# Optimization experiments

Hardware: AMD Instinct MI355X
Metric: run time of the kernel (lower is better)

The kernel has to match this reference:

```python
import jax, jax.numpy as jnp
import numpy as np

NS, B, T, S, H, V, G = 30, 16, 8, 400, 400, 20000, 3


def setup_inputs() -> dict:
    key = jax.random.key(0)
    ks = jax.random.split(key, 16)
    f = lambda k, shp, s: jax.random.normal(k, shp, jnp.float32) * s
    return dict(
        encoded_hidden=f(ks[0], (B, H), 1.0),
        encoded_outputs=f(ks[1], (B, S, H), 1.0),
        slot_emb=f(ks[2], (NS, H), 0.1),
        emb=f(ks[3], (V, H), 0.1),
        W_ih=f(ks[4], (3 * H, H), 0.05),
        W_hh=f(ks[5], (3 * H, H), 0.05),
        b_ih=jnp.zeros((3 * H,), jnp.float32),
        b_hh=jnp.zeros((3 * H,), jnp.float32),
        W_ratio_w=f(ks[6], (1, 3 * H), 0.05),
        W_ratio_b=jnp.zeros((1,), jnp.float32),
        W_gate_w=f(ks[7], (G, H), 0.05),
        W_gate_b=jnp.zeros((G,), jnp.float32),
        story=jax.random.randint(ks[8], (B, S), 0, V),
        target=jax.random.randint(ks[9], (B, NS, T), 0, V),
        encoded_lens=jax.random.randint(ks[10], (B,), S // 2, S + 1).astype(jnp.int32),
    )


def reference(encoded_hidden, encoded_outputs, slot_emb, emb, W_ih, W_hh, b_ih, b_hh,
              W_ratio_w, W_ratio_b, W_gate_w, W_gate_b, story, target, encoded_lens):
    ns, h = slot_emb.shape
    b, s, _ = encoded_outputs.shape
    t = target.shape[2]
    v = emb.shape[0]
    bs = ns * b  # fused slot*batch decode rows (parallel_decode)

    enc_out = jnp.tile(encoded_outputs, (ns, 1, 1))            # [bs,S,H]
    story_r = jnp.tile(story, (ns, 1))                          # [bs,S]
    lens_r = jnp.tile(encoded_lens, (ns,))                      # [bs]
    mask = jnp.arange(s)[None, :] < lens_r[:, None]             # [bs,S]
    h0 = jnp.tile(encoded_hidden, (ns, 1))                      # [bs,H]
    x0 = jnp.broadcast_to(slot_emb[:, None, :], (ns, b, h)).reshape(bs, h)
    # teacher-forcing inputs, slot-major flatten like target[:, :, wi].T.flatten()
    tf_in = emb[jnp.transpose(target, (2, 1, 0)).reshape(t, bs)]  # [T,bs,H]
    row = jnp.arange(bs)[:, None]
    neg_inf = jnp.float32(-jnp.inf)

    def gru_cell(x, hid):
        gi = x @ W_ih.T + b_ih
        gh = hid @ W_hh.T + b_hh
        ir, iz, inn = jnp.split(gi, 3, axis=-1)
        hr, hz, hn = jnp.split(gh, 3, axis=-1)
        r = jax.nn.sigmoid(ir + hr)
        z = jax.nn.sigmoid(iz + hz)
        n = jnp.tanh(inn + r * hn)
        return (1.0 - z) * n + z * hid

    def step(carry, x_next):
        hid, x = carry
        h_new = gru_cell(x, hid)                                # dec_state == hidden for 1-step GRU
        scores = jnp.einsum('bh,bsh->bs', h_new, enc_out)
        scores = jnp.where(mask, scores, neg_inf)
        prob = jax.nn.softmax(scores, axis=1)
        context = jnp.einsum('bs,bsh->bh', prob, enc_out)
        p_vocab = jax.nn.softmax(h_new @ emb.T, axis=1)         # [bs,V]
        p_gen_vec = jnp.concatenate([h_new, context, x], axis=-1)
        switch = jax.nn.sigmoid(p_gen_vec @ W_ratio_w.T + W_ratio_b)  # [bs,1]
        p_ctx = jnp.zeros((bs, v), p_vocab.dtype).at[row, story_r].add(prob)
        final = (1.0 - switch) * p_ctx + switch * p_vocab
        gate = context @ W_gate_w.T + W_gate_b
        return (h_new, x_next), (final, gate)

    _, (finals, gates) = jax.lax.scan(step, (h0, x0), tf_in)
    all_point = finals.reshape(t, ns, b, v).transpose(1, 2, 0, 3)  # [NS,B,T,V]
    all_gate = gates[0].reshape(ns, b, -1)                          # gates from wi==0
    return all_point, all_gate
```

## Files before the change

### kernel.cpp

```cpp
#include <hip/hip_runtime.h>
#include <hip/hip_bf16.h>

#define NSLOT 30
#define BB    16
#define TT    8
#define SS    400
#define HH    400
#define KP    416
#define NKK   13
#define VV    20000
#define GG    3
#define BSR   480
#define NBN   157
#define NCT   1256
#define NG2   1200
#define NCT2  75
#define NRT   30
#define FRAG_STRIDE 512

typedef unsigned short u16;
typedef __attribute__((ext_vector_type(8))) short bf16x8;
typedef __attribute__((ext_vector_type(4))) float f32x4;

__device__ __forceinline__ short f2bfs(float f){
  __hip_bfloat16 h = __float2bfloat16(f);
  union { __hip_bfloat16 b; short u; } v; v.b = h; return v.u;
}
__device__ __forceinline__ unsigned int pack2(float lo, float hi){
  return (unsigned int)(u16)f2bfs(lo) | ((unsigned int)(u16)f2bfs(hi) << 16);
}
__device__ __forceinline__ float bfu(u16 u){
  union { unsigned int i; float f; } v; v.i = ((unsigned int)u) << 16; return v.f;
}
__device__ __forceinline__ float sigm(float x){ return 1.f / (1.f + __expf(-x)); }
__device__ __forceinline__ float tanh_fast(float x){
  float e = __expf(2.f * x);
  return 1.f - 2.f / (e + 1.f);
}
__device__ __forceinline__ float wred_max(float v){
  #pragma unroll
  for (int off = 32; off; off >>= 1) v = fmaxf(v, __shfl_xor(v, off, 64));
  return v;
}
__device__ __forceinline__ float wred_sum(float v){
  #pragma unroll
  for (int off = 32; off; off >>= 1) v += __shfl_xor(v, off, 64);
  return v;
}

__global__ __launch_bounds__(256) void k_init(const float* __restrict__ eh,
                                              const float* __restrict__ semb,
                                              float* __restrict__ h_ws,
                                              float* __restrict__ x_ws)
{
  int idx = blockIdx.x * 256 + threadIdx.x;
  if (idx >= BSR * HH) return;
  int r = idx / HH, k = idx - r * HH;
  int batch = r % BB, slot = r / BB;
  h_ws[idx] = eh[batch * HH + k];
  x_ws[idx] = semb[slot * HH + k];
}

__global__ __launch_bounds__(256) void k_split_xh(
    const float* __restrict__ h_ws, const float* __restrict__ x_ws,
    short* __restrict__ h_hi, short* __restrict__ h_lo,
    short* __restrict__ x_hi, short* __restrict__ x_lo)
{
  const int NU = NRT * NKK * 64;
  for (int u = blockIdx.x * 256 + threadIdx.x; u < 2 * NU; u += gridDim.x * 256){
    int uu = u; int sel = 0;
    if (uu >= NU){ uu -= NU; sel = 1; }
    const float* S = sel ? x_ws : h_ws;
    short* ph = sel ? x_hi : h_hi;
    short* pl = sel ? x_lo : h_lo;
    int lane = uu & 63, kt = uu >> 6;
    int rtile = kt / NKK, kk = kt - rtile * NKK;
    int lg = lane >> 4, rl = lane & 15;
    int r = rtile * 16 + rl, k = kk * 32 + lg * 8;
    bf16x8 oh, ol;
    #pragma unroll
    for (int j = 0; j < 8; ++j){
      if (k + j < HH){
        float v = S[(size_t)r * HH + k + j];
        short hb = f2bfs(v);
        oh[j] = hb; ol[j] = f2bfs(v - bfu((u16)hb));
      } else { oh[j] = 0; ol[j] = 0; }
    }
    *reinterpret_cast<bf16x8*>(ph + (size_t)uu * 8) = oh;
    *reinterpret_cast<bf16x8*>(pl + (size_t)uu * 8) = ol;
  }
}

__global__ __launch_bounds__(256) void k_cast_W(
    const float* __restrict__ Wih, const float* __restrict__ Whh,
    short* __restrict__ Wih_hi, short* __restrict__ Wih_lo,
    short* __restrict__ Whh_hi, short* __restrict__ Whh_lo)
{
  const int NU = NCT2 * NKK * 64;
  for (int u = blockIdx.x * 256 + threadIdx.x; u < 2 * NU; u += gridDim.x * 256){
    int uu = u; int sel = 0;
    if (uu >= NU){ uu -= NU; sel = 1; }
    const float* W = sel ? Whh : Wih;
    short* ph = sel ? Whh_hi : Wih_hi;
    short* pl = sel ? Whh_lo : Wih_lo;
    int lane = uu & 63, kt = uu >> 6;
    int ctile = kt / NKK, kk = kt - ctile * NKK;
    int lg = lane >> 4, cl = lane & 15;
    int c = ctile * 16 + cl, k = kk * 32 + lg * 8;
    bf16x8 oh, ol;
    #pragma unroll
    for (int j = 0; j < 8; ++j){
      if (k + j < HH){
        float v = W[(size_t)c * HH + k + j];
        short hb = f2bfs(v);
        oh[j] = hb; ol[j] = f2bfs(v - bfu((u16)hb));
      } else { oh[j] = 0; ol[j] = 0; }
    }
    *reinterpret_cast<bf16x8*>(ph + (size_t)uu * 8) = oh;
    *reinterpret_cast<bf16x8*>(pl + (size_t)uu * 8) = ol;
  }
}

__global__ __launch_bounds__(256) void k_cast_emb(const float* __restrict__ emb,
                                                  short* __restrict__ ebf)
{
  const int nunit = NCT * NKK * 64;
  for (int u = blockIdx.x * 256 + threadIdx.x; u < nunit; u += gridDim.x * 256){
    int lane = u & 63;
    int kt = u >> 6;
    int ctile = kt / NKK, kk = kt - ctile * NKK;
    int lg = lane >> 4, cl = lane & 15;
    int c = ctile * 16 + cl;
    int k = kk * 32 + lg * 8;
    bf16x8 o;
    if (c < VV && k < HH){
      const float* src = emb + (size_t)c * HH + k;
      #pragma unroll
      for (int j = 0; j < 8; ++j) o[j] = f2bfs(src[j]);
    } else {
      #pragma unroll
      for (int j = 0; j < 8; ++j) o[j] = 0;
    }
    *reinterpret_cast<bf16x8*>(ebf + (size_t)u * 8) = o;
  }
}

__global__ __launch_bounds__(256) void k_gemm2_mfma(
    const short* __restrict__ x_hi, const short* __restrict__ x_lo,
    const short* __restrict__ h_hi, const short* __restrict__ h_lo,
    const short* __restrict__ Wih_hi, const short* __restrict__ Wih_lo,
    const short* __restrict__ Whh_hi, const short* __restrict__ Whh_lo,
    float* __restrict__ gi, float* __restrict__ gh)
{
  const int t = threadIdx.x;
  const int lane = t & 63, wid = t >> 6;
  const int wr = wid >> 1, wc = wid & 1;
  const int l15 = lane & 15, lg = lane >> 4;
  const int bM = blockIdx.x, bN = blockIdx.y, z = blockIdx.z;

  const short* A_hi = z ? h_hi : x_hi;
  const short* A_lo = z ? h_lo : x_lo;
  const short* B_hi = z ? Whh_hi : Wih_hi;
  const short* B_lo = z ? Whh_lo : Wih_lo;
  float* C = z ? gh : gi;

  const short *ah[4], *al[4], *bh[4], *bl[4];
  #pragma unroll
  for (int m = 0; m < 4; ++m){
    int rtile = min(bM * 8 + wr * 4 + m, NRT - 1);
    size_t off = (size_t)rtile * (NKK * FRAG_STRIDE) + lane * 8;
    ah[m] = A_hi + off; al[m] = A_lo + off;
  }
  #pragma unroll
  for (int n = 0; n < 4; ++n){
    int ctile = min(bN * 8 + wc * 4 + n, NCT2 - 1);
    size_t off = (size_t)ctile * (NKK * FRAG_STRIDE) + lane * 8;
    bh[n] = B_hi + off; bl[n] = B_lo + off;
  }

  f32x4 acc[4][4];
  #pragma unroll
  for (int m = 0; m < 4; ++m)
    #pragma unroll
    for (int n = 0; n < 4; ++n)
      acc[m][n] = (f32x4){0.f, 0.f, 0.f, 0.f};

  #pragma unroll
  for (int kk = 0; kk < NKK; ++kk){
    const int ko = kk * FRAG_STRIDE;
    bf16x8 ah_r[4], al_r[4];
    #pragma unroll
    for (int m = 0; m < 4; ++m){
      ah_r[m] = *reinterpret_cast<const bf16x8*>(ah[m] + ko);
      al_r[m] = *reinterpret_cast<const bf16x8*>(al[m] + ko);
    }
    #pragma unroll
    for (int n = 0; n < 4; ++n){
      bf16x8 bhv = *reinterpret_cast<const bf16x8*>(bh[n] + ko);
      bf16x8 blv = *reinterpret_cast<const bf16x8*>(bl[n] + ko);
      #pragma unroll
      for (int m = 0; m < 4; ++m){
        acc[m][n] = __builtin_amdgcn_mfma_f32_16x16x32_bf16(ah_r[m], bhv, acc[m][n], 0, 0, 0);
        acc[m][n] = __builtin_amdgcn_mfma_f32_16x16x32_bf16(ah_r[m], blv, acc[m][n], 0, 0, 0);
        acc[m][n] = __builtin_amdgcn_mfma_f32_16x16x32_bf16(al_r[m], bhv, acc[m][n], 0, 0, 0);
      }
    }
  }

  #pragma unroll
  for (int m = 0; m < 4; ++m){
    #pragma unroll
    for (int q = 0; q < 4; ++q){
      int row = bM * 128 + wr * 64 + m * 16 + lg * 4 + q;
      if (row < BSR){
        #pragma unroll
        for (int n = 0; n < 4; ++n){
          int col = bN * 128 + wc * 64 + n * 16 + l15;
          if (col < NG2) C[(size_t)row * NG2 + col] = acc[m][n][q];
        }
      }
    }
  }
}

__global__ __launch_bounds__(256) void k_logits_mfma(
    const short* __restrict__ hbf, const short* __restrict__ ebf,
    float* __restrict__ out, float* __restrict__ pmax_ws,
    float* __restrict__ psum_ws, int wi)
{
  const int t = threadIdx.x;
  const int lane = t & 63, wid = t >> 6;
  const int wr = wid >> 1, wc = wid & 1;
  const int l15 = lane & 15, lg = lane >> 4;
  const int bM = blockIdx.x, bN = blockIdx.y;

  const short* ap[4];
  const short* bp[4];
  #pragma unroll
  for (int m = 0; m < 4; ++m){
    int rtile = bM * 8 + wr * 4 + m;
    ap[m] = hbf + (size_t)min(rtile, NRT - 1) * (NKK * FRAG_STRIDE) + lane * 8;
  }
  #pragma unroll
  for (int n = 0; n < 4; ++n){
    int ctile = bN * 8 + wc * 4 + n;
    bp[n] = ebf + (size_t)ctile * (NKK * FRAG_STRIDE) + lane * 8;
  }

  f32x4 acc[4][4];
  #pragma unroll
  for (int m = 0; m < 4; ++m)
    #pragma unroll
    for (int n = 0; n < 4; ++n)
      acc[m][n] = (f32x4){0.f, 0.f, 0.f, 0.f};

  #pragma unroll
  for (int kk = 0; kk < NKK; ++kk){
    const int ko = kk * FRAG_STRIDE;
    bf16x8 a[4];
    #pragma unroll
    for (int m = 0; m < 4; ++m)
      a[m] = *reinterpret_cast<const bf16x8*>(ap[m] + ko);
    #pragma unroll
    for (int n = 0; n < 4; ++n){
      bf16x8 b = *reinterpret_cast<const bf16x8*>(bp[n] + ko);
      #pragma unroll
      for (int m = 0; m < 4; ++m)
        acc[m][n] = __builtin_amdgcn_mfma_f32_16x16x32_bf16(a[m], b, acc[m][n], 0, 0, 0);
    }
  }

  #pragma unroll
  for (int m = 0; m < 4; ++m){
    #pragma unroll
    for (int q = 0; q < 4; ++q){
      int row = bM * 128 + wr * 64 + m * 16 + lg * 4 + q;
      u16* lrow16 = reinterpret_cast<u16*>(out + ((size_t)row * TT + wi) * VV);
      #pragma unroll
      for (int n = 0; n < 4; ++n){
        float v = acc[m][n][q];
        float vp = __shfl_xor(v, 1, 64);
        int col = bN * 128 + wc * 64 + n * 16 + l15;
        if (((l15 & 1) == 0) && row < BSR && col < VV)
          *reinterpret_cast<unsigned int*>(lrow16 + col) = pack2(v, vp);
      }
    }
    f32x4 rmax, rsum;
    #pragma unroll
    for (int q = 0; q < 4; ++q){
      float mx = -3.0e38f;
      #pragma unroll
      for (int n = 0; n < 4; ++n){
        int col = bN * 128 + wc * 64 + n * 16 + l15;
        float v = (col < VV) ? acc[m][n][q] : -3.0e38f;
        mx = fmaxf(mx, v);
      }
      #pragma unroll
      for (int off = 1; off < 16; off <<= 1) mx = fmaxf(mx, __shfl_xor(mx, off, 64));
      float sm = 0.f;
      #pragma unroll
      for (int n = 0; n < 4; ++n){
        int col = bN * 128 + wc * 64 + n * 16 + l15;
        if (col < VV) sm += __expf(acc[m][n][q] - mx);
      }
      #pragma unroll
      for (int off = 1; off < 16; off <<= 1) sm += __shfl_xor(sm, off, 64);
      rmax[q] = mx; rsum[q] = sm;
    }
    if (l15 == 0){
      #pragma unroll
      for (int q = 0; q < 4; ++q){
        int row = bM * 128 + wr * 64 + m * 16 + lg * 4 + q;
        if (row < BSR){
          size_t pidx = ((size_t)row * NBN + bN) * 2 + wc;
          pmax_ws[pidx] = rmax[q];
          psum_ws[pidx] = rsum[q];
        }
      }
    }
  }
}

__global__ __launch_bounds__(256) void k_att(
    const float* __restrict__ enc, const float* __restrict__ emb,
    const float* __restrict__ b_ih, const float* __restrict__ b_hh,
    const float* __restrict__ Wr_w, const float* __restrict__ Wr_b,
    const float* __restrict__ Wg_w, const float* __restrict__ Wg_b,
    const int* __restrict__ target, const int* __restrict__ lens,
    const float* __restrict__ gi_ws, const float* __restrict__ gh_ws,
    float* __restrict__ h_ws, float* __restrict__ x_ws,
    short* __restrict__ h_hi, short* __restrict__ h_lo,
    short* __restrict__ x_hi, short* __restrict__ x_lo,
    float* __restrict__ prob_ws, float* __restrict__ sw_ws,
    float* __restrict__ d_out, int wi)
{
  __shared__ float hn_s[HH];
  __shared__ float sc_s[SS];
  __shared__ float ctx_s[HH];
  __shared__ float red[4];
  __shared__ float redg[GG][4];

  const int t = threadIdx.x;
  const int rg = blockIdx.x;
  const int batch = rg % BB, slot = rg / BB;
  const int len = lens[batch];
  const int rtile = rg >> 4, rl = rg & 15;

  const float* gir = gi_ws + (size_t)rg * NG2;
  const float* ghr = gh_ws + (size_t)rg * NG2;
  for (int k = t; k < HH; k += 256){
    float irv = gir[k]          + b_ih[k];
    float izv = gir[HH + k]     + b_ih[HH + k];
    float inv = gir[2 * HH + k] + b_ih[2 * HH + k];
    float hrv = ghr[k]          + b_hh[k];
    float hzv = ghr[HH + k]     + b_hh[HH + k];
    float hnv = ghr[2 * HH + k] + b_hh[2 * HH + k];
    float rr = sigm(irv + hrv);
    float zz = sigm(izv + hzv);
    float nn = tanh_fast(inv + rr * hnv);
    float hold = h_ws[(size_t)rg * HH + k];
    float hnew = (1.f - zz) * nn + zz * hold;
    hn_s[k] = hnew;
    h_ws[(size_t)rg * HH + k] = hnew;
  }
  __syncthreads();

  if (t < KP / 8){
    const int kk = t >> 2, lg = t & 3;
    bf16x8 oh, ol;
    #pragma unroll
    for (int j = 0; j < 8; ++j){
      int k = t * 8 + j;
      if (k < HH){
        float v = hn_s[k];
        short hb = f2bfs(v);
        oh[j] = hb; ol[j] = f2bfs(v - bfu((u16)hb));
      } else { oh[j] = 0; ol[j] = 0; }
    }
    size_t off = ((size_t)rtile * NKK + kk) * FRAG_STRIDE + (lg * 16 + rl) * 8;
    *reinterpret_cast<bf16x8*>(h_hi + off) = oh;
    *reinterpret_cast<bf16x8*>(h_lo + off) = ol;
  }

  const float* encb = enc + (size_t)batch * SS * HH;
  float lmax = -3.0e38f;
  for (int s = t; s < SS; s += 256){
    if (s < len){
      const float4* er4 = reinterpret_cast<const float4*>(encb + (size_t)s * HH);
      float dot = 0.f;
      for (int k4 = 0; k4 < HH / 4; ++k4){
        float4 e = er4[k4];
        float4 hv = *reinterpret_cast<const float4*>(&hn_s[k4 * 4]);
        dot += e.x*hv.x + e.y*hv.y + e.z*hv.z + e.w*hv.w;
      }
      sc_s[s] = dot;
      lmax = fmaxf(lmax, dot);
    }
  }
  lmax = wred_max(lmax);
  if ((t & 63) == 0) red[t >> 6] = lmax;
  __syncthreads();
  lmax = fmaxf(fmaxf(red[0], red[1]), fmaxf(red[2], red[3]));
  float lsum = 0.f;
  for (int s = t; s < SS; s += 256){
    float e = (s < len) ? __expf(sc_s[s] - lmax) : 0.f;
    sc_s[s] = e;
    lsum += e;
  }
  lsum = wred_sum(lsum);
  __syncthreads();
  if ((t & 63) == 0) red[t >> 6] = lsum;
  __syncthreads();
  lsum = red[0] + red[1] + red[2] + red[3];
  float invl = 1.f / lsum;
  for (int s = t; s < SS; s += 256){
    float p = sc_s[s] * invl;
    sc_s[s] = p;
    prob_ws[(size_t)rg * SS + s] = p;
  }
  __syncthreads();

  for (int k = t; k < HH; k += 256){
    float c0 = 0.f, c1 = 0.f, c2 = 0.f, c3 = 0.f;
    const float* ek = encb + k;
    int s = 0;
    for (; s + 3 < len; s += 4){
      c0 += sc_s[s]     * ek[(size_t)s * HH];
      c1 += sc_s[s + 1] * ek[(size_t)(s + 1) * HH];
      c2 += sc_s[s + 2] * ek[(size_t)(s + 2) * HH];
      c3 += sc_s[s + 3] * ek[(size_t)(s + 3) * HH];
    }
    for (; s < len; ++s) c0 += sc_s[s] * ek[(size_t)s * HH];
    ctx_s[k] = (c0 + c1) + (c2 + c3);
  }
  __syncthreads();

  float sa = 0.f;
  for (int k = t; k < HH; k += 256){
    sa += Wr_w[k]          * hn_s[k]
        + Wr_w[HH + k]     * ctx_s[k]
        + Wr_w[2 * HH + k] * x_ws[(size_t)rg * HH + k];
  }
  sa = wred_sum(sa);
  if ((t & 63) == 0) red[t >> 6] = sa;
  __syncthreads();
  sa = red[0] + red[1] + red[2] + red[3];
  if (t == 0) sw_ws[rg] = sigm(sa + Wr_b[0]);

  if (wi == 0){
    float ga[GG] = {0.f, 0.f, 0.f};
    for (int k = t; k < HH; k += 256){
      float cv = ctx_s[k];
      ga[0] += Wg_w[k] * cv;
      ga[1] += Wg_w[HH + k] * cv;
      ga[2] += Wg_w[2 * HH + k] * cv;
    }
    #pragma unroll
    for (int g = 0; g < GG; ++g){
      ga[g] = wred_sum(ga[g]);
      if ((t & 63) == 0) redg[g][t >> 6] = ga[g];
    }
    __syncthreads();
    if (t < GG)
      d_out[(size_t)NSLOT * BB * TT * VV + (size_t)rg * GG + t] =
          redg[t][0] + redg[t][1] + redg[t][2] + redg[t][3] + Wg_b[t];
  }

  const int tgt = target[batch * (NSLOT * TT) + slot * TT + wi];
  const float* embrow = emb + (size_t)tgt * HH;
  for (int k = t; k < HH; k += 256)
    x_ws[(size_t)rg * HH + k] = embrow[k];
  if (t < KP / 8){
    const int kk = t >> 2, lg = t & 3;
    bf16x8 oh, ol;
    #pragma unroll
    for (int j = 0; j < 8; ++j){
      int k = t * 8 + j;
      if (k < HH){
        float v = embrow[k];
        short hb = f2bfs(v);
        oh[j] = hb; ol[j] = f2bfs(v - bfu((u16)hb));
      } else { oh[j] = 0; ol[j] = 0; }
    }
    size_t off = ((size_t)rtile * NKK + kk) * FRAG_STRIDE + (lg * 16 + rl) * 8;
    *reinterpret_cast<bf16x8*>(x_hi + off) = oh;
    *reinterpret_cast<bf16x8*>(x_lo + off) = ol;
  }
}

__global__ __launch_bounds__(256) void k_finalize(
    float* __restrict__ logits_out, const float* __restrict__ prob_ws,
    const float* __restrict__ pmax_ws, const float* __restrict__ psum_ws,
    const float* __restrict__ sw_ws, const int* __restrict__ story,
    const int* __restrict__ lens, int wi)
{
  __shared__ float pctx[VV];
  __shared__ u16 rowbuf[VV];
  __shared__ float red[4];
  const int t = threadIdx.x;
  const int r = blockIdx.x;
  const int batch = r % BB;
  for (int v = t; v < VV; v += 256) pctx[v] = 0.f;
  __syncthreads();
  const int len = lens[batch];
  for (int s = t; s < SS; s += 256){
    if (s < len)
      atomicAdd(&pctx[story[batch * SS + s]], prob_ws[(size_t)r * SS + s]);
  }

  float* lrow = logits_out + ((size_t)r * TT + wi) * VV;
  const uint4* l16 = reinterpret_cast<const uint4*>(lrow);
  for (int i = t; i < VV / 8; i += 256)
    reinterpret_cast<uint4*>(rowbuf)[i] = l16[i];

  const float* pm = pmax_ws + (size_t)r * (NBN * 2);
  const float* ps = psum_ws + (size_t)r * (NBN * 2);
  float m = -3.0e38f;
  for (int i = t; i < NBN * 2; i += 256) m = fmaxf(m, pm[i]);
  m = wred_max(m);
  if ((t & 63) == 0) red[t >> 6] = m;
  __syncthreads();
  m = fmaxf(fmaxf(red[0], red[1]), fmaxf(red[2], red[3]));
  float lsum = 0.f;
  for (int i = t; i < NBN * 2; i += 256) lsum += ps[i] * __expf(pm[i] - m);
  lsum = wred_sum(lsum);
  __syncthreads();
  if ((t & 63) == 0) red[t >> 6] = lsum;
  __syncthreads();
  lsum = red[0] + red[1] + red[2] + red[3];

  const float sw = sw_ws[r];
  const float invl = sw / lsum;
  const float osw = 1.f - sw;
  float4* o4 = reinterpret_cast<float4*>(lrow);
  for (int i = t; i < VV / 4; i += 256){
    ushort4 s4 = reinterpret_cast<const ushort4*>(rowbuf)[i];
    int v = i * 4;
    float4 o;
    o.x = __expf(bfu(s4.x) - m) * invl + osw * pctx[v + 0];
    o.y = __expf(bfu(s4.y) - m) * invl + osw * pctx[v + 1];
    o.z = __expf(bfu(s4.z) - m) * invl + osw * pctx[v + 2];
    o.w = __expf(bfu(s4.w) - m) * invl + osw * pctx[v + 3];
    o4[i] = o;
  }
}

extern "C" void kernel_launch(void* const* d_in, const int* in_sizes, int n_in,
                              void* d_out, int out_size, void* d_ws, size_t ws_size,
                              hipStream_t stream)
{
  (void)in_sizes; (void)n_in; (void)out_size; (void)ws_size;
  const float* eh    = (const float*)d_in[0];
  const float* enc   = (const float*)d_in[1];
  const float* semb  = (const float*)d_in[2];
  const float* emb   = (const float*)d_in[3];
  const float* W_ih  = (const float*)d_in[4];
  const float* W_hh  = (const float*)d_in[5];
  const float* b_ih  = (const float*)d_in[6];
  const float* b_hh  = (const float*)d_in[7];
  const float* Wr_w  = (const float*)d_in[8];
  const float* Wr_b  = (const float*)d_in[9];
  const float* Wg_w  = (const float*)d_in[10];
  const float* Wg_b  = (const float*)d_in[11];
  const int* story = (const int*)d_in[12];
  const int* tgt   = (const int*)d_in[13];
  const int* lens  = (const int*)d_in[14];
  float* out = (float*)d_out;

  float* ws      = (float*)d_ws;
  float* h_ws    = ws;
  float* x_ws    = ws + 192000;
  float* prob_ws = ws + 384000;
  float* sw_ws   = ws + 576000;
  float* gi_ws   = ws + 576512;
  float* gh_ws   = ws + 1152512;
  float* pmax_ws = ws + 1728512;
  float* psum_ws = ws + 1879552;
  short* h_hi    = (short*)(ws + 2030592);
  short* emb_bf  = (short*)(ws + 2130432);
  short* Wih_hi  = (short*)(ws + 6310400);
  short* Wih_lo  = (short*)(ws + 6560000);
  short* Whh_hi  = (short*)(ws + 6809600);
  short* Whh_lo  = (short*)(ws + 7059200);
  short* x_hi    = (short*)(ws + 7308800);
  short* x_lo    = (short*)(ws + 7408640);
  short* h_lo    = (short*)(ws + 7508480);

  k_cast_emb<<<2048, 256, 0, stream>>>(emb, emb_bf);
  k_cast_W<<<512, 256, 0, stream>>>(W_ih, W_hh, Wih_hi, Wih_lo, Whh_hi, Whh_lo);
  k_init<<<750, 256, 0, stream>>>(eh, semb, h_ws, x_ws);
  k_split_xh<<<195, 256, 0, stream>>>(h_ws, x_ws, h_hi, h_lo, x_hi, x_lo);
  for (int wi = 0; wi < TT; ++wi){
    dim3 gg(4, 10, 2);
    k_gemm2_mfma<<<gg, 256, 0, stream>>>(x_hi, x_lo, h_hi, h_lo,
                                         Wih_hi, Wih_lo, Whh_hi, Whh_lo,
                                         gi_ws, gh_ws);
    k_att<<<BSR, 256, 0, stream>>>(enc, emb, b_ih, b_hh, Wr_w, Wr_b, Wg_w, Wg_b,
                                   tgt, lens, gi_ws, gh_ws, h_ws, x_ws,
                                   h_hi, h_lo, x_hi, x_lo,
                                   prob_ws, sw_ws, out, wi);
    dim3 gl(4, NBN);
    k_logits_mfma<<<gl, 256, 0, stream>>>(h_hi, emb_bf, out, pmax_ws, psum_ws, wi);
    k_finalize<<<BSR, 256, 0, stream>>>(out, prob_ws, pmax_ws, psum_ws,
                                        sw_ws, story, lens, wi);
  }
}
```

Baseline: 1.017 ms.

## Cast encoder outputs to bf16 and split finalize into dense and scatter passes

Encoder outputs are converted once to bf16, and the attention kernel reads the bf16 copy for both the score and context loops, halving the bytes streamed from enc each step. The finalize kernel is split in two. The first writes the scaled vocab softmax without the 80KB shared pctx buffer, which should raise occupancy. The second scatters the copy-distribution probabilities into the output row with global atomics. In exchange, attention precision drops to bf16, there is one more launch per step, and a one-time cast kernel is added.

```diff
diff --git a/kernel.cpp b/kernel.cpp
--- a/kernel.cpp
+++ b/kernel.cpp
@@ -32,6 +32,12 @@
 __device__ __forceinline__ float bfu(u16 u){
   union { unsigned int i; float f; } v; v.i = ((unsigned int)u) << 16; return v.f;
 }
+__device__ __forceinline__ float bfu_lo(unsigned int u){
+  union { unsigned int i; float f; } v; v.i = u << 16; return v.f;
+}
+__device__ __forceinline__ float bfu_hi(unsigned int u){
+  union { unsigned int i; float f; } v; v.i = u & 0xffff0000u; return v.f;
+}
 __device__ __forceinline__ float sigm(float x){ return 1.f / (1.f + __expf(-x)); }
 __device__ __forceinline__ float tanh_fast(float x){
   float e = __expf(2.f * x);
@@ -59,6 +65,14 @@
   int batch = r % BB, slot = r / BB;
   h_ws[idx] = eh[batch * HH + k];
   x_ws[idx] = semb[slot * HH + k];
+}
+
+__global__ __launch_bounds__(256) void k_cast_enc(const float* __restrict__ enc,
+                                                  u16* __restrict__ enc_bf)
+{
+  const int n = BB * SS * HH;
+  for (int i = blockIdx.x * 256 + threadIdx.x; i < n; i += gridDim.x * 256)
+    enc_bf[i] = (u16)f2bfs(enc[i]);
 }
 
 __global__ __launch_bounds__(256) void k_split_xh(
@@ -322,7 +336,7 @@
 }
 
 __global__ __launch_bounds__(256) void k_att(
-    const float* __restrict__ enc, const float* __restrict__ emb,
+    const u16* __restrict__ enc_bf, const float* __restrict__ emb,
     const float* __restrict__ b_ih, const float* __restrict__ b_hh,
     const float* __restrict__ Wr_w, const float* __restrict__ Wr_b,
     const float* __restrict__ Wg_w, const float* __restrict__ Wg_b,
@@ -382,16 +396,19 @@
     *reinterpret_cast<bf16x8*>(h_lo + off) = ol;
   }
 
-  const float* encb = enc + (size_t)batch * SS * HH;
+  const u16* encb = enc_bf + (size_t)batch * SS * HH;
   float lmax = -3.0e38f;
   for (int s = t; s < SS; s += 256){
     if (s < len){
-      const float4* er4 = reinterpret_cast<const float4*>(encb + (size_t)s * HH);
+      const uint4* er4 = reinterpret_cast<const uint4*>(encb + (size_t)s * HH);
       float dot = 0.f;
-      for (int k4 = 0; k4 < HH / 4; ++k4){
-        float4 e = er4[k4];
-        float4 hv = *reinterpret_cast<const float4*>(&hn_s[k4 * 4]);
-        dot += e.x*hv.x + e.y*hv.y + e.z*hv.z + e.w*hv.w;
+      for (int k8 = 0; k8 < HH / 8; ++k8){
+        uint4 e = er4[k8];
+        const float* hv = &hn_s[k8 * 8];
+        dot += bfu_lo(e.x)*hv[0] + bfu_hi(e.x)*hv[1]
+             + bfu_lo(e.y)*hv[2] + bfu_hi(e.y)*hv[3]
+             + bfu_lo(e.z)*hv[4] + bfu_hi(e.z)*hv[5]
+             + bfu_lo(e.w)*hv[6] + bfu_hi(e.w)*hv[7];
       }
       sc_s[s] = dot;
       lmax = fmaxf(lmax, dot);
@@ -422,15 +439,15 @@
 
   for (int k = t; k < HH; k += 256){
     float c0 = 0.f, c1 = 0.f, c2 = 0.f, c3 = 0.f;
-    const float* ek = encb + k;
+    const u16* ek = encb + k;
     int s = 0;
     for (; s + 3 < len; s += 4){
-      c0 += sc_s[s]     * ek[(size_t)s * HH];
-      c1 += sc_s[s + 1] * ek[(size_t)(s + 1) * HH];
-      c2 += sc_s[s + 2] * ek[(size_t)(s + 2) * HH];
-      c3 += sc_s[s + 3] * ek[(size_t)(s + 3) * HH];
-    }
-    for (; s < len; ++s) c0 += sc_s[s] * ek[(size_t)s * HH];
+      c0 += sc_s[s]     * bfu(ek[(size_t)s * HH]);
+      c1 += sc_s[s + 1] * bfu(ek[(size_t)(s + 1) * HH]);
+      c2 += sc_s[s + 2] * bfu(ek[(size_t)(s + 2) * HH]);
+      c3 += sc_s[s + 3] * bfu(ek[(size_t)(s + 3) * HH]);
+    }
+    for (; s < len; ++s) c0 += sc_s[s] * bfu(ek[(size_t)s * HH]);
     ctx_s[k] = (c0 + c1) + (c2 + c3);
   }
   __syncthreads();
@@ -488,25 +505,15 @@
   }
 }
 
-__global__ __launch_bounds__(256) void k_finalize(
-    float* __restrict__ logits_out, const float* __restrict__ prob_ws,
+__global__ __launch_bounds__(256) void k_fin1(
+    float* __restrict__ logits_out,
     const float* __restrict__ pmax_ws, const float* __restrict__ psum_ws,
-    const float* __restrict__ sw_ws, const int* __restrict__ story,
-    const int* __restrict__ lens, int wi)
-{
-  __shared__ float pctx[VV];
+    const float* __restrict__ sw_ws, int wi)
+{
   __shared__ u16 rowbuf[VV];
   __shared__ float red[4];
   const int t = threadIdx.x;
   const int r = blockIdx.x;
-  const int batch = r % BB;
-  for (int v = t; v < VV; v += 256) pctx[v] = 0.f;
-  __syncthreads();
-  const int len = lens[batch];
-  for (int s = t; s < SS; s += 256){
-    if (s < len)
-      atomicAdd(&pctx[story[batch * SS + s]], prob_ws[(size_t)r * SS + s]);
-  }
 
   float* lrow = logits_out + ((size_t)r * TT + wi) * VV;
   const uint4* l16 = reinterpret_cast<const uint4*>(lrow);
@@ -529,20 +536,31 @@
   __syncthreads();
   lsum = red[0] + red[1] + red[2] + red[3];
 
-  const float sw = sw_ws[r];
-  const float invl = sw / lsum;
-  const float osw = 1.f - sw;
+  const float invl = sw_ws[r] / lsum;
   float4* o4 = reinterpret_cast<float4*>(lrow);
   for (int i = t; i < VV / 4; i += 256){
     ushort4 s4 = reinterpret_cast<const ushort4*>(rowbuf)[i];
-    int v = i * 4;
     float4 o;
-    o.x = __expf(bfu(s4.x) - m) * invl + osw * pctx[v + 0];
-    o.y = __expf(bfu(s4.y) - m) * invl + osw * pctx[v + 1];
-    o.z = __expf(bfu(s4.z) - m) * invl + osw * pctx[v + 2];
-    o.w = __expf(bfu(s4.w) - m) * invl + osw * pctx[v + 3];
+    o.x = __expf(bfu(s4.x) - m) * invl;
+    o.y = __expf(bfu(s4.y) - m) * invl;
+    o.z = __expf(bfu(s4.z) - m) * invl;
+    o.w = __expf(bfu(s4.w) - m) * invl;
     o4[i] = o;
   }
+}
+
+__global__ __launch_bounds__(128) void k_fin2(
+    float* __restrict__ logits_out, const float* __restrict__ prob_ws,
+    const float* __restrict__ sw_ws, const int* __restrict__ story,
+    const int* __restrict__ lens, int wi)
+{
+  const int r = blockIdx.x, t = threadIdx.x;
+  const int batch = r % BB;
+  const int len = lens[batch];
+  const float osw = 1.f - sw_ws[r];
+  float* lrow = logits_out + ((size_t)r * TT + wi) * VV;
+  for (int s = t; s < len; s += 128)
+    atomicAdd(&lrow[story[batch * SS + s]], osw * prob_ws[(size_t)r * SS + s]);
 }
 
 extern "C" void kernel_launch(void* const* d_in, const int* in_sizes, int n_in,
@@ -585,9 +603,11 @@
   short* x_hi    = (short*)(ws + 7308800);
   short* x_lo    = (short*)(ws + 7408640);
   short* h_lo    = (short*)(ws + 7508480);
+  u16*   enc_bf  = (u16*)(ws + 7608320);
 
   k_cast_emb<<<2048, 256, 0, stream>>>(emb, emb_bf);
   k_cast_W<<<512, 256, 0, stream>>>(W_ih, W_hh, Wih_hi, Wih_lo, Whh_hi, Whh_lo);
+  k_cast_enc<<<2048, 256, 0, stream>>>(enc, enc_bf);
   k_init<<<750, 256, 0, stream>>>(eh, semb, h_ws, x_ws);
   k_split_xh<<<195, 256, 0, stream>>>(h_ws, x_ws, h_hi, h_lo, x_hi, x_lo);
   for (int wi = 0; wi < TT; ++wi){
@@ -595,13 +615,13 @@
     k_gemm2_mfma<<<gg, 256, 0, stream>>>(x_hi, x_lo, h_hi, h_lo,
                                          Wih_hi, Wih_lo, Whh_hi, Whh_lo,
                                          gi_ws, gh_ws);
-    k_att<<<BSR, 256, 0, stream>>>(enc, emb, b_ih, b_hh, Wr_w, Wr_b, Wg_w, Wg_b,
+    k_att<<<BSR, 256, 0, stream>>>(enc_bf, emb, b_ih, b_hh, Wr_w, Wr_b, Wg_w, Wg_b,
                                    tgt, lens, gi_ws, gh_ws, h_ws, x_ws,
                                    h_hi, h_lo, x_hi, x_lo,
                                    prob_ws, sw_ws, out, wi);
     dim3 gl(4, NBN);
     k_logits_mfma<<<gl, 256, 0, stream>>>(h_hi, emb_bf, out, pmax_ws, psum_ws, wi);
-    k_finalize<<<BSR, 256, 0, stream>>>(out, prob_ws, pmax_ws, psum_ws,
-                                        sw_ws, story, lens, wi);
-  }
-}
+    k_fin1<<<BSR, 256, 0, stream>>>(out, pmax_ws, psum_ws, sw_ws, wi);
+    k_fin2<<<BSR, 128, 0, stream>>>(out, prob_ws, sw_ws, story, lens, wi);
+  }
+}
```

Result: no change. 1.034 ms (+1.6%).

## Move attention score computation to split-bf16 MFMA kernel, split GRU from attention

Applied to the files above, without the earlier changes.

The attention kernel is split into three stages: a GRU elementwise kernel that also writes the new hidden state in a second per-batch fragment layout, a batched MFMA score kernel that computes h·enc per batch with three-term hi/lo bf16 products, and an attention kernel that reads precomputed scores. The encoder outputs are pre-split into hi/lo bf16 MFMA fragments once up front. This replaces the per-row scalar FP32 dot products over S×H, which re-read encoder rows for every slot, with matrix-core work that shares encoder tiles across the 30 slots. In exchange it adds two kernel launches per step and a scratch buffer aliased onto gi_ws, and the scores carry slightly less precision than FP32.

```diff
diff --git a/kernel.cpp b/kernel.cpp
--- a/kernel.cpp
+++ b/kernel.cpp
@@ -16,6 +16,7 @@
 #define NG2   1200
 #define NCT2  75
 #define NRT   30
+#define NST   25
 #define FRAG_STRIDE 512
 
 typedef unsigned short u16;
@@ -64,7 +65,8 @@
 __global__ __launch_bounds__(256) void k_split_xh(
     const float* __restrict__ h_ws, const float* __restrict__ x_ws,
     short* __restrict__ h_hi, short* __restrict__ h_lo,
-    short* __restrict__ x_hi, short* __restrict__ x_lo)
+    short* __restrict__ x_hi, short* __restrict__ x_lo,
+    short* __restrict__ h2_hi, short* __restrict__ h2_lo)
 {
   const int NU = NRT * NKK * 64;
   for (int u = blockIdx.x * 256 + threadIdx.x; u < 2 * NU; u += gridDim.x * 256){
@@ -88,6 +90,13 @@
     }
     *reinterpret_cast<bf16x8*>(ph + (size_t)uu * 8) = oh;
     *reinterpret_cast<bf16x8*>(pl + (size_t)uu * 8) = ol;
+    if (!sel){
+      int slot = r >> 4, batch = r & 15;
+      size_t o2 = ((size_t)(batch * 2 + (slot >> 4)) * NKK + kk) * FRAG_STRIDE
+                + (lg * 16 + (slot & 15)) * 8;
+      *reinterpret_cast<bf16x8*>(h2_hi + o2) = oh;
+      *reinterpret_cast<bf16x8*>(h2_lo + o2) = ol;
+    }
   }
 }
 
@@ -145,6 +154,33 @@
   }
 }
 
+__global__ __launch_bounds__(256) void k_cast_encA(const float* __restrict__ enc,
+                                                   short* __restrict__ eA_hi,
+                                                   short* __restrict__ eA_lo)
+{
+  const int NU = BB * NST * NKK * 64;
+  for (int u = blockIdx.x * 256 + threadIdx.x; u < NU; u += gridDim.x * 256){
+    int lane = u & 63, kt = u >> 6;
+    int kk = kt % NKK; int ct = kt / NKK;
+    int stile = ct % NST; int b = ct / NST;
+    int lg = lane >> 4, cl = lane & 15;
+    int s = stile * 16 + cl;
+    int kh = kk * 32 + lg * 8;
+    bf16x8 oh, ol;
+    const float* src = enc + ((size_t)b * SS + s) * HH;
+    #pragma unroll
+    for (int j = 0; j < 8; ++j){
+      if (kh + j < HH){
+        float v = src[kh + j];
+        short hb = f2bfs(v);
+        oh[j] = hb; ol[j] = f2bfs(v - bfu((u16)hb));
+      } else { oh[j] = 0; ol[j] = 0; }
+    }
+    *reinterpret_cast<bf16x8*>(eA_hi + (size_t)u * 8) = oh;
+    *reinterpret_cast<bf16x8*>(eA_lo + (size_t)u * 8) = ol;
+  }
+}
+
 __global__ __launch_bounds__(256) void k_gemm2_mfma(
     const short* __restrict__ x_hi, const short* __restrict__ x_lo,
     const short* __restrict__ h_hi, const short* __restrict__ h_lo,
@@ -223,132 +259,21 @@
   }
 }
 
-__global__ __launch_bounds__(256) void k_logits_mfma(
-    const short* __restrict__ hbf, const short* __restrict__ ebf,
-    float* __restrict__ out, float* __restrict__ pmax_ws,
-    float* __restrict__ psum_ws, int wi)
-{
-  const int t = threadIdx.x;
-  const int lane = t & 63, wid = t >> 6;
-  const int wr = wid >> 1, wc = wid & 1;
-  const int l15 = lane & 15, lg = lane >> 4;
-  const int bM = blockIdx.x, bN = blockIdx.y;
-
-  const short* ap[4];
-  const short* bp[4];
-  #pragma unroll
-  for (int m = 0; m < 4; ++m){
-    int rtile = bM * 8 + wr * 4 + m;
-    ap[m] = hbf + (size_t)min(rtile, NRT - 1) * (NKK * FRAG_STRIDE) + lane * 8;
-  }
-  #pragma unroll
-  for (int n = 0; n < 4; ++n){
-    int ctile = bN * 8 + wc * 4 + n;
-    bp[n] = ebf + (size_t)ctile * (NKK * FRAG_STRIDE) + lane * 8;
-  }
-
-  f32x4 acc[4][4];
-  #pragma unroll
-  for (int m = 0; m < 4; ++m)
-    #pragma unroll
-    for (int n = 0; n < 4; ++n)
-      acc[m][n] = (f32x4){0.f, 0.f, 0.f, 0.f};
-
-  #pragma unroll
-  for (int kk = 0; kk < NKK; ++kk){
-    const int ko = kk * FRAG_STRIDE;
-    bf16x8 a[4];
-    #pragma unroll
-    for (int m = 0; m < 4; ++m)
-      a[m] = *reinterpret_cast<const bf16x8*>(ap[m] + ko);
-    #pragma unroll
-    for (int n = 0; n < 4; ++n){
-      bf16x8 b = *reinterpret_cast<const bf16x8*>(bp[n] + ko);
-      #pragma unroll
-      for (int m = 0; m < 4; ++m)
-        acc[m][n] = __builtin_amdgcn_mfma_f32_16x16x32_bf16(a[m], b, acc[m][n], 0, 0, 0);
-    }
-  }
-
-  #pragma unroll
-  for (int m = 0; m < 4; ++m){
-    #pragma unroll
-    for (int q = 0; q < 4; ++q){
-      int row = bM * 128 + wr * 64 + m * 16 + lg * 4 + q;
-      u16* lrow16 = reinterpret_cast<u16*>(out + ((size_t)row * TT + wi) * VV);
-      #pragma unroll
-      for (int n = 0; n < 4; ++n){
-        float v = acc[m][n][q];
-        float vp = __shfl_xor(v, 1, 64);
-        int col = bN * 128 + wc * 64 + n * 16 + l15;
-        if (((l15 & 1) == 0) && row < BSR && col < VV)
-          *reinterpret_cast<unsigned int*>(lrow16 + col) = pack2(v, vp);
-      }
-    }
-    f32x4 rmax, rsum;
-    #pragma unroll
-    for (int q = 0; q < 4; ++q){
-      float mx = -3.0e38f;
-      #pragma unroll
-      for (int n = 0; n < 4; ++n){
-        int col = bN * 128 + wc * 64 + n * 16 + l15;
-        float v = (col < VV) ? acc[m][n][q] : -3.0e38f;
-        mx = fmaxf(mx, v);
-      }
-      #pragma unroll
-      for (int off = 1; off < 16; off <<= 1) mx = fmaxf(mx, __shfl_xor(mx, off, 64));
-      float sm = 0.f;
-      #pragma unroll
-      for (int n = 0; n < 4; ++n){
-        int col = bN * 128 + wc * 64 + n * 16 + l15;
-        if (col < VV) sm += __expf(acc[m][n][q] - mx);
-      }
-      #pragma unroll
-      for (int off = 1; off < 16; off <<= 1) sm += __shfl_xor(sm, off, 64);
-      rmax[q] = mx; rsum[q] = sm;
-    }
-    if (l15 == 0){
-      #pragma unroll
-      for (int q = 0; q < 4; ++q){
-        int row = bM * 128 + wr * 64 + m * 16 + lg * 4 + q;
-        if (row < BSR){
-          size_t pidx = ((size_t)row * NBN + bN) * 2 + wc;
-          pmax_ws[pidx] = rmax[q];
-          psum_ws[pidx] = rsum[q];
-        }
-      }
-    }
-  }
-}
-
-__global__ __launch_bounds__(256) void k_att(
-    const float* __restrict__ enc, const float* __restrict__ emb,
+__global__ __launch_bounds__(128) void k_gru(
+    const float* __restrict__ gi_ws, const float* __restrict__ gh_ws,
     const float* __restrict__ b_ih, const float* __restrict__ b_hh,
-    const float* __restrict__ Wr_w, const float* __restrict__ Wr_b,
-    const float* __restrict__ Wg_w, const float* __restrict__ Wg_b,
-    const int* __restrict__ target, const int* __restrict__ lens,
-    const float* __restrict__ gi_ws, const float* __restrict__ gh_ws,
-    float* __restrict__ h_ws, float* __restrict__ x_ws,
+    float* __restrict__ h_ws,
     short* __restrict__ h_hi, short* __restrict__ h_lo,
-    short* __restrict__ x_hi, short* __restrict__ x_lo,
-    float* __restrict__ prob_ws, float* __restrict__ sw_ws,
-    float* __restrict__ d_out, int wi)
+    short* __restrict__ h2_hi, short* __restrict__ h2_lo)
 {
   __shared__ float hn_s[HH];
-  __shared__ float sc_s[SS];
-  __shared__ float ctx_s[HH];
-  __shared__ float red[4];
-  __shared__ float redg[GG][4];
-
   const int t = threadIdx.x;
   const int rg = blockIdx.x;
-  const int batch = rg % BB, slot = rg / BB;
-  const int len = lens[batch];
-  const int rtile = rg >> 4, rl = rg & 15;
+  const int slot = rg >> 4, batch = rg & 15;
 
   const float* gir = gi_ws + (size_t)rg * NG2;
   const float* ghr = gh_ws + (size_t)rg * NG2;
-  for (int k = t; k < HH; k += 256){
+  for (int k = t; k < HH; k += 128){
     float irv = gir[k]          + b_ih[k];
     float izv = gir[HH + k]     + b_ih[HH + k];
     float inv = gir[2 * HH + k] + b_ih[2 * HH + k];
@@ -377,25 +302,100 @@
         oh[j] = hb; ol[j] = f2bfs(v - bfu((u16)hb));
       } else { oh[j] = 0; ol[j] = 0; }
     }
-    size_t off = ((size_t)rtile * NKK + kk) * FRAG_STRIDE + (lg * 16 + rl) * 8;
-    *reinterpret_cast<bf16x8*>(h_hi + off) = oh;
-    *reinterpret_cast<bf16x8*>(h_lo + off) = ol;
-  }
-
-  const float* encb = enc + (size_t)batch * SS * HH;
+    size_t o1 = ((size_t)slot * NKK + kk) * FRAG_STRIDE + (lg * 16 + batch) * 8;
+    *reinterpret_cast<bf16x8*>(h_hi + o1) = oh;
+    *reinterpret_cast<bf16x8*>(h_lo + o1) = ol;
+    size_t o2 = ((size_t)(batch * 2 + (slot >> 4)) * NKK + kk) * FRAG_STRIDE
+              + (lg * 16 + (slot & 15)) * 8;
+    *reinterpret_cast<bf16x8*>(h2_hi + o2) = oh;
+    *reinterpret_cast<bf16x8*>(h2_lo + o2) = ol;
+  }
+}
+
+__global__ __launch_bounds__(256) void k_score(
+    const short* __restrict__ h2_hi, const short* __restrict__ h2_lo,
+    const short* __restrict__ eA_hi, const short* __restrict__ eA_lo,
+    float* __restrict__ sc_ws)
+{
+  const int t = threadIdx.x;
+  const int lane = t & 63, wid = t >> 6;
+  const int wr = wid >> 1, wc = wid & 1;
+  const int l15 = lane & 15, lg = lane >> 4;
+  const int b = blockIdx.x, sc = blockIdx.y;
+
+  const short *ah, *al;
+  {
+    size_t off = ((size_t)(b * 2 + wr) * NKK) * FRAG_STRIDE + lane * 8;
+    ah = h2_hi + off; al = h2_lo + off;
+  }
+  const short *bh[4], *bl[4];
+  #pragma unroll
+  for (int n = 0; n < 4; ++n){
+    int stile = min(sc * 8 + wc * 4 + n, NST - 1);
+    size_t off = ((size_t)(b * NST + stile) * NKK) * FRAG_STRIDE + lane * 8;
+    bh[n] = eA_hi + off; bl[n] = eA_lo + off;
+  }
+
+  f32x4 acc[4];
+  #pragma unroll
+  for (int n = 0; n < 4; ++n) acc[n] = (f32x4){0.f, 0.f, 0.f, 0.f};
+
+  #pragma unroll
+  for (int kk = 0; kk < NKK; ++kk){
+    const int ko = kk * FRAG_STRIDE;
+    bf16x8 ahv = *reinterpret_cast<const bf16x8*>(ah + ko);
+    bf16x8 alv = *reinterpret_cast<const bf16x8*>(al + ko);
+    #pragma unroll
+    for (int n = 0; n < 4; ++n){
+      bf16x8 bhv = *reinterpret_cast<const bf16x8*>(bh[n] + ko);
+      bf16x8 blv = *reinterpret_cast<const bf16x8*>(bl[n] + ko);
+      acc[n] = __builtin_amdgcn_mfma_f32_16x16x32_bf16(ahv, bhv, acc[n], 0, 0, 0);
+      acc[n] = __builtin_amdgcn_mfma_f32_16x16x32_bf16(ahv, blv, acc[n], 0, 0, 0);
+      acc[n] = __builtin_amdgcn_mfma_f32_16x16x32_bf16(alv, bhv, acc[n], 0, 0, 0);
+    }
+  }
+
+  #pragma unroll
+  for (int q = 0; q < 4; ++q){
+    int slot = wr * 16 + lg * 4 + q;
+    #pragma unroll
+    for (int n = 0; n < 4; ++n){
+      int s = sc * 128 + wc * 64 + n * 16 + l15;
+      if (s < SS)
+        sc_ws[((size_t)b * 32 + slot) * 512 + s] = acc[n][q];
+    }
+  }
+}
+
+__global__ __launch_bounds__(256) void k_att2(
+    const float* __restrict__ enc, const float* __restrict__ emb,
+    const float* __restrict__ Wr_w, const float* __restrict__ Wr_b,
+    const float* __restrict__ Wg_w, const float* __restrict__ Wg_b,
+    const int* __restrict__ target, const int* __restrict__ lens,
+    const float* __restrict__ sc_ws, const float* __restrict__ h_ws,
+    float* __restrict__ x_ws,
+    short* __restrict__ x_hi, short* __restrict__ x_lo,
+    float* __restrict__ prob_ws, float* __restrict__ sw_ws,
+    float* __restrict__ d_out, int wi)
+{
+  __shared__ float hn_s[HH];
+  __shared__ float sc_s[SS];
+  __shared__ float ctx_s[HH];
+  __shared__ float red[4];
+  __shared__ float redg[GG][4];
+
+  const int t = threadIdx.x;
+  const int rg = blockIdx.x;
+  const int batch = rg % BB, slot = rg / BB;
+  const int len = lens[batch];
+
+  for (int k = t; k < HH; k += 256) hn_s[k] = h_ws[(size_t)rg * HH + k];
+  const float* scrow = sc_ws + ((size_t)batch * 32 + slot) * 512;
   float lmax = -3.0e38f;
   for (int s = t; s < SS; s += 256){
-    if (s < len){
-      const float4* er4 = reinterpret_cast<const float4*>(encb + (size_t)s * HH);
-      float dot = 0.f;
-      for (int k4 = 0; k4 < HH / 4; ++k4){
-        float4 e = er4[k4];
-        float4 hv = *reinterpret_cast<const float4*>(&hn_s[k4 * 4]);
-        dot += e.x*hv.x + e.y*hv.y + e.z*hv.z + e.w*hv.w;
-      }
-      sc_s[s] = dot;
-      lmax = fmaxf(lmax, dot);
-    }
+    float v = scrow[s];
+    sc_s[s] = v;
+    if (s < len) lmax = fmaxf(lmax, v);
   }
   lmax = wred_max(lmax);
   if ((t & 63) == 0) red[t >> 6] = lmax;
@@ -420,6 +420,7 @@
   }
   __syncthreads();
 
+  const float* encb = enc + (size_t)batch * SS * HH;
   for (int k = t; k < HH; k += 256){
     float c0 = 0.f, c1 = 0.f, c2 = 0.f, c3 = 0.f;
     const float* ek = encb + k;
@@ -482,9 +483,107 @@
         oh[j] = hb; ol[j] = f2bfs(v - bfu((u16)hb));
       } else { oh[j] = 0; ol[j] = 0; }
     }
-    size_t off = ((size_t)rtile * NKK + kk) * FRAG_STRIDE + (lg * 16 + rl) * 8;
+    size_t off = ((size_t)slot * NKK + kk) * FRAG_STRIDE + (lg * 16 + batch) * 8;
     *reinterpret_cast<bf16x8*>(x_hi + off) = oh;
     *reinterpret_cast<bf16x8*>(x_lo + off) = ol;
+  }
+}
+
+__global__ __launch_bounds__(256) void k_logits_mfma(
+    const short* __restrict__ hbf, const short* __restrict__ ebf,
+    float* __restrict__ out, float* __restrict__ pmax_ws,
+    float* __restrict__ psum_ws, int wi)
+{
+  const int t = threadIdx.x;
+  const int lane = t & 63, wid = t >> 6;
+  const int wr = wid >> 1, wc = wid & 1;
+  const int l15 = lane & 15, lg = lane >> 4;
+  const int bM = blockIdx.x, bN = blockIdx.y;
+
+  const short* ap[4];
+  const short* bp[4];
+  #pragma unroll
+  for (int m = 0; m < 4; ++m){
+    int rtile = bM * 8 + wr * 4 + m;
+    ap[m] = hbf + (size_t)min(rtile, NRT - 1) * (NKK * FRAG_STRIDE) + lane * 8;
+  }
+  #pragma unroll
+  for (int n = 0; n < 4; ++n){
+    int ctile = bN * 8 + wc * 4 + n;
+    bp[n] = ebf + (size_t)ctile * (NKK * FRAG_STRIDE) + lane * 8;
+  }
+
+  f32x4 acc[4][4];
+  #pragma unroll
+  for (int m = 0; m < 4; ++m)
+    #pragma unroll
+    for (int n = 0; n < 4; ++n)
+      acc[m][n] = (f32x4){0.f, 0.f, 0.f, 0.f};
+
+  #pragma unroll
+  for (int kk = 0; kk < NKK; ++kk){
+    const int ko = kk * FRAG_STRIDE;
+    bf16x8 a[4];
+    #pragma unroll
+    for (int m = 0; m < 4; ++m)
+      a[m] = *reinterpret_cast<const bf16x8*>(ap[m] + ko);
+    #pragma unroll
+    for (int n = 0; n < 4; ++n){
+      bf16x8 b = *reinterpret_cast<const bf16x8*>(bp[n] + ko);
+      #pragma unroll
+      for (int m = 0; m < 4; ++m)
+        acc[m][n] = __builtin_amdgcn_mfma_f32_16x16x32_bf16(a[m], b, acc[m][n], 0, 0, 0);
+    }
+  }
+
+  #pragma unroll
+  for (int m = 0; m < 4; ++m){
+    #pragma unroll
+    for (int q = 0; q < 4; ++q){
+      int row = bM * 128 + wr * 64 + m * 16 + lg * 4 + q;
+      u16* lrow16 = reinterpret_cast<u16*>(out + ((size_t)row * TT + wi) * VV);
+      #pragma unroll
+      for (int n = 0; n < 4; ++n){
+        float v = acc[m][n][q];
+        float vp = __shfl_xor(v, 1, 64);
+        int col = bN * 128 + wc * 64 + n * 16 + l15;
+        if (((l15 & 1) == 0) && row < BSR && col < VV)
+          *reinterpret_cast<unsigned int*>(lrow16 + col) = pack2(v, vp);
+      }
+    }
+    f32x4 rmax, rsum;
+    #pragma unroll
+    for (int q = 0; q < 4; ++q){
+      float mx = -3.0e38f;
+      #pragma unroll
+      for (int n = 0; n < 4; ++n){
+        int col = bN * 128 + wc * 64 + n * 16 + l15;
+        float v = (col < VV) ? acc[m][n][q] : -3.0e38f;
+        mx = fmaxf(mx, v);
+      }
+      #pragma unroll
+      for (int off = 1; off < 16; off <<= 1) mx = fmaxf(mx, __shfl_xor(mx, off, 64));
+      float sm = 0.f;
+      #pragma unroll
+      for (int n = 0; n < 4; ++n){
+        int col = bN * 128 + wc * 64 + n * 16 + l15;
+        if (col < VV) sm += __expf(acc[m][n][q] - mx);
+      }
+      #pragma unroll
+      for (int off = 1; off < 16; off <<= 1) sm += __shfl_xor(sm, off, 64);
+      rmax[q] = mx; rsum[q] = sm;
+    }
+    if (l15 == 0){
+      #pragma unroll
+      for (int q = 0; q < 4; ++q){
+        int row = bM * 128 + wr * 64 + m * 16 + lg * 4 + q;
+        if (row < BSR){
+          size_t pidx = ((size_t)row * NBN + bN) * 2 + wc;
+          pmax_ws[pidx] = rmax[q];
+          psum_ws[pidx] = rsum[q];
+        }
+      }
+    }
   }
 }
 
@@ -585,20 +684,30 @@
   short* x_hi    = (short*)(ws + 7308800);
   short* x_lo    = (short*)(ws + 7408640);
   short* h_lo    = (short*)(ws + 7508480);
+  short* h2_hi   = (short*)(ws + 7608320);
+  short* h2_lo   = (short*)(ws + 7714816);
+  short* eA_hi   = (short*)(ws + 7821312);
+  short* eA_lo   = (short*)(ws + 9152512);
+  float* sc_ws   = gi_ws;
 
   k_cast_emb<<<2048, 256, 0, stream>>>(emb, emb_bf);
   k_cast_W<<<512, 256, 0, stream>>>(W_ih, W_hh, Wih_hi, Wih_lo, Whh_hi, Whh_lo);
+  k_cast_encA<<<1024, 256, 0, stream>>>(enc, eA_hi, eA_lo);
   k_init<<<750, 256, 0, stream>>>(eh, semb, h_ws, x_ws);
-  k_split_xh<<<195, 256, 0, stream>>>(h_ws, x_ws, h_hi, h_lo, x_hi, x_lo);
+  k_split_xh<<<195, 256, 0, stream>>>(h_ws, x_ws, h_hi, h_lo, x_hi, x_lo,
+                                      h2_hi, h2_lo);
   for (int wi = 0; wi < TT; ++wi){
     dim3 gg(4, 10, 2);
     k_gemm2_mfma<<<gg, 256, 0, stream>>>(x_hi, x_lo, h_hi, h_lo,
                                          Wih_hi, Wih_lo, Whh_hi, Whh_lo,
                                          gi_ws, gh_ws);
-    k_att<<<BSR, 256, 0, stream>>>(enc, emb, b_ih, b_hh, Wr_w, Wr_b, Wg_w, Wg_b,
-                                   tgt, lens, gi_ws, gh_ws, h_ws, x_ws,
-                                   h_hi, h_lo, x_hi, x_lo,
-                                   prob_ws, sw_ws, out, wi);
+    k_gru<<<BSR, 128, 0, stream>>>(gi_ws, gh_ws, b_ih, b_hh, h_ws,
+                                   h_hi, h_lo, h2_hi, h2_lo);
+    dim3 gs(16, 4);
+    k_score<<<gs, 256, 0, stream>>>(h2_hi, h2_lo, eA_hi, eA_lo, sc_ws);
+    k_att2<<<BSR, 256, 0, stream>>>(enc, emb, Wr_w, Wr_b, Wg_w, Wg_b,
+                                    tgt, lens, sc_ws, h_ws, x_ws,
+                                    x_hi, x_lo, prob_ws, sw_ws, out, wi);
     dim3 gl(4, NBN);
     k_logits_mfma<<<gl, 256, 0, stream>>>(h_hi, emb_bf, out, pmax_ws, psum_ws, wi);
     k_finalize<<<BSR, 256, 0, stream>>>(out, prob_ws, pmax_ws, psum_ws,
```

New measurement: 1.142 ms. 12.3% more time.
